# Kernel optimization log

Measured on AMD Instinct MI355X. Metric: run time of the kernel, lower is better.

The kernel has to match this reference:

```python
import jax, jax.numpy as jnp
import numpy as np

N_NODES = 50000
D_FEAT = 128
HIDDEN = 256
CLASSES = 40
N_EDGES = 800000


def setup_inputs() -> dict:
    key = jax.random.key(0)
    ks = jax.random.split(key, 8)
    x = jax.random.normal(ks[0], (N_NODES, D_FEAT), dtype=jnp.float32)
    edge_index = jax.random.randint(ks[1], (2, N_EDGES), 0, N_NODES, dtype=jnp.int64)
    s1 = 1.0 / np.sqrt(D_FEAT)
    s2 = 1.0 / np.sqrt(HIDDEN)
    # PyG SAGEConv: lin_l (applied to aggregated neighbors, has bias), lin_r (root, no bias)
    Wl1 = jax.random.uniform(ks[2], (HIDDEN, D_FEAT), jnp.float32, -s1, s1)
    bl1 = jnp.zeros((HIDDEN,), jnp.float32)
    Wr1 = jax.random.uniform(ks[3], (HIDDEN, D_FEAT), jnp.float32, -s1, s1)
    Wl2 = jax.random.uniform(ks[4], (CLASSES, HIDDEN), jnp.float32, -s2, s2)
    bl2 = jnp.zeros((CLASSES,), jnp.float32)
    Wr2 = jax.random.uniform(ks[5], (CLASSES, HIDDEN), jnp.float32, -s2, s2)
    return {"x": x, "edge_index": edge_index, "Wl1": Wl1, "bl1": bl1, "Wr1": Wr1,
            "Wl2": Wl2, "bl2": bl2, "Wr2": Wr2}


def _mean_aggregate(x, src, dst, n_nodes):
    # gather source features along edges, scatter-mean into destinations
    summed = jax.ops.segment_sum(x[src], dst, num_segments=n_nodes)  # [N, d]
    counts = jax.ops.segment_sum(jnp.ones((src.shape[0],), x.dtype), dst,
                                 num_segments=n_nodes)
    return summed / jnp.maximum(counts, 1.0)[:, None]


def _sage_conv(x, src, dst, Wl, bl, Wr):
    agg = _mean_aggregate(x, src, dst, x.shape[0])
    return agg @ Wl.T + bl + x @ Wr.T


def reference(x, edge_index, Wl1, bl1, Wr1, Wl2, bl2, Wr2):
    src, dst = edge_index[0], edge_index[1]
    h = _sage_conv(x, src, dst, Wl1, bl1, Wr1)
    h = jax.nn.relu(h)
    # F.dropout(training=self.training): eval-mode inference -> identity
    h = _sage_conv(h, src, dst, Wl2, bl2, Wr2)
    return jax.nn.log_softmax(h, axis=1)
```

## Files before the change

### kernel.cpp

```cpp
#include <hip/hip_runtime.h>
#include <hip/hip_bf16.h>
#include <math.h>

#define N_NODES 50000
#define D_FEAT  128
#define HIDDEN  256
#define CLASSES 40
#define N_EDGES 800000
#define P2S 64
#define R2S 48
#define HLS 264
#define ALS 136
#define NTILES 3125
#define GRID_L 512
#define NBUCK 196
#define BCAP  5120
#define XCVT_BLOCKS 6250
#define BA_BLOCKS 784
#define WCVT_BLOCKS 336
#define FRONT_BLOCKS (XCVT_BLOCKS + BA_BLOCKS + WCVT_BLOCKS)

typedef unsigned int  u32;
typedef unsigned short u16;
typedef __attribute__((ext_vector_type(8))) short short8;
typedef __attribute__((ext_vector_type(4))) float floatx4;

__device__ __forceinline__ float bf_lo(u32 w) { union { u32 i; float f; } u; u.i = w << 16; return u.f; }
__device__ __forceinline__ float bf_hi(u32 w) { union { u32 i; float f; } u; u.i = w & 0xffff0000u; return u.f; }
__device__ __forceinline__ float bf1(u16 h)   { union { u32 i; float f; } u; u.i = ((u32)h) << 16; return u.f; }
__device__ __forceinline__ u16 f2bf(float f) {
  union { float f; u32 i; } u; u.f = f; u32 i = u.i;
  return (u16)((i + 0x7fffu + ((i >> 16) & 1u)) >> 16);
}
__device__ __forceinline__ u32 packbf(float a, float b) { return (u32)f2bf(a) | ((u32)f2bf(b) << 16); }

__device__ __forceinline__ bool edges_are_i64(const void* eraw) {
  const long long* p = (const long long*)eraw;
  bool ok = true;
  #pragma unroll
  for (int i = 0; i < 8; i++) {
    long long v = p[(size_t)i * 100003];
    ok = ok && (v >= 0) && (v < N_NODES);
  }
  return ok;
}

__global__ __launch_bounds__(256) void front_kernel(
    const float* __restrict__ x, u16* __restrict__ xb,
    const void* __restrict__ eraw, int* __restrict__ bcur, u32* __restrict__ bbuf,
    const float* __restrict__ Wl1, const float* __restrict__ Wr1,
    const float* __restrict__ Wl2, const float* __restrict__ Wr2,
    u16* __restrict__ wb) {
  const int t = threadIdx.x;
  if (blockIdx.x < XCVT_BLOCKS) {
    int i = (blockIdx.x * 256 + t) * 4;
    floatx4 v = *(const floatx4*)(x + i);
    u32* o = (u32*)(xb + i);
    o[0] = packbf(v.x, v.y);
    o[1] = packbf(v.z, v.w);
    return;
  }
  if (blockIdx.x >= XCVT_BLOCKS + BA_BLOCKS) {
    int i = (blockIdx.x - XCVT_BLOCKS - BA_BLOCKS) * 256 + t;
    if (i < 32768)      wb[i] = f2bf(Wl1[i]);
    else if (i < 65536) wb[i] = f2bf(Wr1[i - 32768]);
    else if (i < 75776) wb[i] = f2bf(Wl2[i - 65536]);
    else if (i < 86016) wb[i] = f2bf(Wr2[i - 75776]);
    return;
  }
  __shared__ int hist[NBUCK], base[NBUCK], loc[NBUCK];
  const bool i64f = edges_are_i64(eraw);
  const int eb = blockIdx.x - XCVT_BLOCKS;
  for (int i = t; i < NBUCK; i += 256) { hist[i] = 0; loc[i] = 0; }
  __syncthreads();

  int sreg[4], dreg[4];
  const int e0 = eb * 1024;
  #pragma unroll
  for (int j = 0; j < 4; j++) {
    int e = e0 + j * 256 + t;
    int ss = 0, dd = -1;
    if (e < N_EDGES) {
      if (i64f) {
        const long long* p = (const long long*)eraw;
        ss = (int)p[e]; dd = (int)p[N_EDGES + e];
      } else {
        const int* p = (const int*)eraw;
        ss = p[e]; dd = p[N_EDGES + e];
      }
      if ((u32)ss >= N_NODES || (u32)dd >= N_NODES) dd = -1;
    }
    sreg[j] = ss; dreg[j] = dd;
    if (dd >= 0) atomicAdd(&hist[dd >> 8], 1);
  }
  __syncthreads();
  for (int i = t; i < NBUCK; i += 256)
    base[i] = atomicAdd(&bcur[i], hist[i]);
  __syncthreads();
  #pragma unroll
  for (int j = 0; j < 4; j++) {
    int dd = dreg[j];
    if (dd >= 0) {
      int bk = dd >> 8;
      int pos = base[bk] + atomicAdd(&loc[bk], 1);
      if (pos < BCAP)
        bbuf[(size_t)bk * BCAP + pos] = (u32)sreg[j] | ((u32)(dd & 255) << 16);
    }
  }
}

__global__ __launch_bounds__(256) void bucketBC_kernel(
    const u32* __restrict__ bbuf, const int* __restrict__ bcur,
    int* __restrict__ offsets, int* __restrict__ csr) {
  __shared__ int cnt[256];
  __shared__ int lds[256];
  const int t = threadIdx.x;
  const int b = blockIdx.x;
  int c196 = (t < NBUCK) ? min(bcur[t], BCAP) : 0;
  lds[t] = c196;
  __syncthreads();
  #pragma unroll
  for (int d = 1; d < 256; d <<= 1) {
    int v = (t >= d) ? lds[t - d] : 0;
    __syncthreads();
    lds[t] += v;
    __syncthreads();
  }
  const int btop = (b > 0) ? lds[b - 1] : 0;
  if (b == NBUCK - 1 && t == 0) offsets[N_NODES] = lds[NBUCK - 1];
  cnt[t] = 0;
  __syncthreads();
  const int n = min(bcur[b], BCAP);
  for (int i = t; i < n; i += 256) {
    u32 e = bbuf[(size_t)b * BCAP + i];
    atomicAdd(&cnt[(e >> 16) & 255], 1);
  }
  __syncthreads();
  int c = cnt[t];
  lds[t] = c;
  __syncthreads();
  #pragma unroll
  for (int d = 1; d < 256; d <<= 1) {
    int v = (t >= d) ? lds[t - d] : 0;
    __syncthreads();
    lds[t] += v;
    __syncthreads();
  }
  const int node = b * 256 + t;
  const int off = lds[t] - c + btop;
  if (node < N_NODES) offsets[node] = off;
  cnt[t] = off;
  __syncthreads();
  for (int i = t; i < n; i += 256) {
    u32 e = bbuf[(size_t)b * BCAP + i];
    int dl = (e >> 16) & 255;
    int pos = atomicAdd(&cnt[dl], 1);
    csr[pos] = (int)(e & 0xFFFFu);
  }
}

__global__ __launch_bounds__(256) void gather1_kernel(
    const u16* __restrict__ xb, const int* __restrict__ offsets,
    const int* __restrict__ csr_src, u16* __restrict__ agg1) {
  const int node = blockIdx.x * 4 + (threadIdx.x >> 6);
  const int lane = threadIdx.x & 63;
  int b = offsets[node], e = offsets[node + 1];
  float a0 = 0.f, a1 = 0.f, b0 = 0.f, b1 = 0.f;
  float c0 = 0.f, c1 = 0.f, d0 = 0.f, d1 = 0.f;
  float e0 = 0.f, e1 = 0.f, f0 = 0.f, f1 = 0.f;
  float g0 = 0.f, g1 = 0.f, h0 = 0.f, h1 = 0.f;
  int i = b;
  for (; i + 8 <= e; i += 8) {
    int s0 = csr_src[i],     s1 = csr_src[i + 1], s2 = csr_src[i + 2], s3 = csr_src[i + 3];
    int s4 = csr_src[i + 4], s5 = csr_src[i + 5], s6 = csr_src[i + 6], s7 = csr_src[i + 7];
    u32 w0 = ((const u32*)(xb + (size_t)s0 * D_FEAT))[lane];
    u32 w1 = ((const u32*)(xb + (size_t)s1 * D_FEAT))[lane];
    u32 w2 = ((const u32*)(xb + (size_t)s2 * D_FEAT))[lane];
    u32 w3 = ((const u32*)(xb + (size_t)s3 * D_FEAT))[lane];
    u32 w4 = ((const u32*)(xb + (size_t)s4 * D_FEAT))[lane];
    u32 w5 = ((const u32*)(xb + (size_t)s5 * D_FEAT))[lane];
    u32 w6 = ((const u32*)(xb + (size_t)s6 * D_FEAT))[lane];
    u32 w7 = ((const u32*)(xb + (size_t)s7 * D_FEAT))[lane];
    a0 += bf_lo(w0); a1 += bf_hi(w0);
    b0 += bf_lo(w1); b1 += bf_hi(w1);
    c0 += bf_lo(w2); c1 += bf_hi(w2);
    d0 += bf_lo(w3); d1 += bf_hi(w3);
    e0 += bf_lo(w4); e1 += bf_hi(w4);
    f0 += bf_lo(w5); f1 += bf_hi(w5);
    g0 += bf_lo(w6); g1 += bf_hi(w6);
    h0 += bf_lo(w7); h1 += bf_hi(w7);
  }
  for (; i < e; i++) {
    int s = csr_src[i];
    u32 w = ((const u32*)(xb + (size_t)s * D_FEAT))[lane];
    a0 += bf_lo(w); a1 += bf_hi(w);
  }
  float s0 = ((a0 + b0) + (c0 + d0)) + ((e0 + f0) + (g0 + h0));
  float s1 = ((a1 + b1) + (c1 + d1)) + ((e1 + f1) + (g1 + h1));
  float inv = 1.0f / (float)max(e - b, 1);
  ((u32*)(agg1 + (size_t)node * D_FEAT))[lane] = packbf(s0 * inv, s1 * inv);
}

__global__ __launch_bounds__(256, 2) void layer_kernel(
    const u16* __restrict__ agg1, const u16* __restrict__ xb,
    const u16* __restrict__ Wl1b, const u16* __restrict__ Wr1b,
    const float* __restrict__ bl1,
    const u16* __restrict__ Wl2b, const u16* __restrict__ Wr2b,
    const float* __restrict__ bl2,
    u16* __restrict__ p2b, float* __restrict__ r2f) {
  __shared__ u16 h_lds[16 * HLS];
  __shared__ u16 a_lds[16 * ALS];
  __shared__ u16 x_lds[16 * ALS];
  const int lane = threadIdx.x & 63;
  const int wave = threadIdx.x >> 6;
  const int n15  = lane & 15;
  const int quad = lane >> 4;
  const int ko   = quad * 8;
  const int colbase = wave * 64;
  const int srow = (wave << 2) + quad;
  const int scol = n15 * 8;

  short8 Bf[8][4];
  #pragma unroll
  for (int s = 0; s < 8; s++) {
    const u16* W = (s < 4) ? Wl1b : Wr1b;
    const int kk = (s & 3) * 32;
    #pragma unroll
    for (int t = 0; t < 4; t++)
      Bf[s][t] = *(const short8*)(W + (size_t)(colbase + t * 16 + n15) * D_FEAT + ko + kk);
  }

  const int  c0   = wave;
  const bool isR0 = (c0 >= 3);
  const int  tc0  = c0 - (isR0 ? 3 : 0);
  const int  wr0  = min(tc0 * 16 + n15, CLASSES - 1);
  const u16* Wc0  = (isR0 ? Wr2b : Wl2b) + (size_t)wr0 * HIDDEN + ko;
  const bool has1 = (wave < 2);
  const int  tc1  = wave + 1;
  const int  wr1  = min(tc1 * 16 + n15, CLASSES - 1);
  const u16* Wc1  = Wr2b + (size_t)wr1 * HIDDEN + ko;

  const float bias0 = bl2[min(tc0 * 16 + n15, CLASSES - 1)];
  const float bias1 = bl2[min(tc1 * 16 + n15, CLASSES - 1)];

  for (int tile = blockIdx.x; tile < NTILES; tile += GRID_L) {
    const int m0 = tile * 16;
    {
      const size_t g = (size_t)(m0 + srow) * D_FEAT + scol;
      *(short8*)(a_lds + srow * ALS + scol) = *(const short8*)(agg1 + g);
      *(short8*)(x_lds + srow * ALS + scol) = *(const short8*)(xb + g);
    }
    __syncthreads();
    {
      floatx4 acc[4];
      #pragma unroll
      for (int t = 0; t < 4; t++) acc[t] = floatx4{0.f, 0.f, 0.f, 0.f};

      short8 a[4];
      #pragma unroll
      for (int s = 0; s < 4; s++) a[s] = *(const short8*)(a_lds + n15 * ALS + ko + s * 32);
      #pragma unroll
      for (int s = 0; s < 4; s++)
        #pragma unroll
        for (int t = 0; t < 4; t++)
          acc[t] = __builtin_amdgcn_mfma_f32_16x16x32_bf16(a[s], Bf[s][t], acc[t], 0, 0, 0);
      #pragma unroll
      for (int s = 0; s < 4; s++) a[s] = *(const short8*)(x_lds + n15 * ALS + ko + s * 32);
      #pragma unroll
      for (int s = 0; s < 4; s++)
        #pragma unroll
        for (int t = 0; t < 4; t++)
          acc[t] = __builtin_amdgcn_mfma_f32_16x16x32_bf16(a[s], Bf[4 + s][t], acc[t], 0, 0, 0);

      #pragma unroll
      for (int t = 0; t < 4; t++) {
        int col = colbase + t * 16 + n15;
        float bias = bl1[col];
        #pragma unroll
        for (int r = 0; r < 4; r++) {
          float v = acc[t][r] + bias;
          v = v > 0.f ? v : 0.f;
          h_lds[(quad * 4 + r) * HLS + col] = f2bf(v);
        }
      }
    }
    __syncthreads();
    {
      floatx4 acc0 = floatx4{0.f, 0.f, 0.f, 0.f};
      floatx4 acc1 = floatx4{0.f, 0.f, 0.f, 0.f};
      #pragma unroll
      for (int s = 0; s < 8; s++) {
        short8 a2 = *(const short8*)(&h_lds[n15 * HLS + s * 32 + ko]);
        acc0 = __builtin_amdgcn_mfma_f32_16x16x32_bf16(a2, *(const short8*)(Wc0 + s * 32), acc0, 0, 0, 0);
        if (has1)
          acc1 = __builtin_amdgcn_mfma_f32_16x16x32_bf16(a2, *(const short8*)(Wc1 + s * 32), acc1, 0, 0, 0);
      }
      {
        int col = tc0 * 16 + n15;
        #pragma unroll
        for (int r = 0; r < 4; r++) {
          int row = m0 + quad * 4 + r;
          if (isR0) r2f[(size_t)row * R2S + col] = acc0[r] + bias0;
          else      p2b[(size_t)row * P2S + col] = f2bf(acc0[r]);
        }
      }
      if (has1) {
        int col = tc1 * 16 + n15;
        #pragma unroll
        for (int r = 0; r < 4; r++) {
          int row = m0 + quad * 4 + r;
          r2f[(size_t)row * R2S + col] = acc1[r] + bias1;
        }
      }
    }
    __syncthreads();
  }
}

__global__ __launch_bounds__(256) void final_kernel(
    const u16* __restrict__ p2b, const float* __restrict__ r2f,
    const int* __restrict__ offsets, const int* __restrict__ csr_src,
    float* __restrict__ out) {
  const int node  = blockIdx.x * 4 + (threadIdx.x >> 6);
  const int lane  = threadIdx.x & 63;
  const int eslot = lane >> 5;
  const int k     = lane & 31;
  const u32* p2w  = (const u32*)p2b;
  int b = offsets[node], e = offsets[node + 1];
  float slo = 0.f, shi = 0.f;
  int i = b;
  for (; i + 16 <= e; i += 16) {
    int c[8];
    #pragma unroll
    for (int j = 0; j < 8; j++) c[j] = csr_src[i + 2 * j + eslot];
    u32 w[8];
    #pragma unroll
    for (int j = 0; j < 8; j++) w[j] = p2w[((u32)c[j] << 5) + k];
    #pragma unroll
    for (int j = 0; j < 8; j++) { slo += bf_lo(w[j]); shi += bf_hi(w[j]); }
  }
  for (; i + 2 <= e; i += 2) {
    int c = csr_src[i + eslot];
    u32 w = p2w[((u32)c << 5) + k];
    slo += bf_lo(w); shi += bf_hi(w);
  }
  if (i < e && eslot == 0) {
    int c = csr_src[i];
    u32 w = p2w[((u32)c << 5) + k];
    slo += bf_lo(w); shi += bf_hi(w);
  }
  slo += __shfl_xor(slo, 32, 64);
  shi += __shfl_xor(shi, 32, 64);
  float vlo = __shfl(slo, lane >> 1, 64);
  float vhi = __shfl(shi, lane >> 1, 64);
  float ssum = (lane & 1) ? vhi : vlo;
  float inv = 1.0f / (float)max(e - b, 1);
  const bool act = (lane < CLASSES);
  float v = act ? (ssum * inv + r2f[(size_t)node * R2S + lane]) : -INFINITY;
  float mx = v;
  #pragma unroll
  for (int d = 1; d < 64; d <<= 1) mx = fmaxf(mx, __shfl_xor(mx, d, 64));
  float ex = act ? expf(v - mx) : 0.f;
  float sum = ex;
  #pragma unroll
  for (int d = 1; d < 64; d <<= 1) sum += __shfl_xor(sum, d, 64);
  float l = mx + logf(sum);
  if (act) out[(size_t)node * CLASSES + lane] = v - l;
}

extern "C" void kernel_launch(void* const* d_in, const int* in_sizes, int n_in,
                              void* d_out, int out_size, void* d_ws, size_t ws_size,
                              hipStream_t stream) {
  const float* x   = (const float*)d_in[0];
  const void*  ei  = d_in[1];
  const float* Wl1 = (const float*)d_in[2];
  const float* bl1 = (const float*)d_in[3];
  const float* Wr1 = (const float*)d_in[4];
  const float* Wl2 = (const float*)d_in[5];
  const float* bl2 = (const float*)d_in[6];
  const float* Wr2 = (const float*)d_in[7];

  char* ws = (char*)d_ws;
  size_t off = 0;
  int* csr       = (int*)(ws + off); off += (size_t)N_EDGES * 4;
  int* offsets   = (int*)(ws + off); off += 204800;
  int* bcur      = (int*)(ws + off); off += 1024;
  u32* bbuf      = (u32*)(ws + off); off += (size_t)NBUCK * BCAP * 4;
  u16* wb        = (u16*)(ws + off); off += 172288;
  u16* xb        = (u16*)(ws + off); off += (size_t)N_NODES * D_FEAT * 2;
  u16* agg1      = (u16*)(ws + off); off += (size_t)N_NODES * D_FEAT * 2;
  u16* p2b       = (u16*)(ws + off); off += (size_t)N_NODES * P2S * 2;
  float* r2f     = (float*)(ws + off); off += (size_t)N_NODES * R2S * 4;

  u16* Wl1b = wb;
  u16* Wr1b = wb + 32768;
  u16* Wl2b = wb + 65536;
  u16* Wr2b = wb + 75776;

  hipMemsetAsync(bcur, 0, NBUCK * 4, stream);
  front_kernel<<<FRONT_BLOCKS, 256, 0, stream>>>(x, xb, ei, bcur, bbuf,
                                                 Wl1, Wr1, Wl2, Wr2, wb);
  bucketBC_kernel<<<NBUCK, 256, 0, stream>>>(bbuf, bcur, offsets, csr);
  gather1_kernel<<<N_NODES / 4, 256, 0, stream>>>(xb, offsets, csr, agg1);
  layer_kernel<<<GRID_L, 256, 0, stream>>>(agg1, xb, Wl1b, Wr1b, bl1,
                                           Wl2b, Wr2b, bl2, p2b, r2f);
  final_kernel<<<N_NODES / 4, 256, 0, stream>>>(p2b, r2f, offsets, csr, (float*)d_out);
}
```

Measured before the change: 220.7 us.

## Split layer-2 projection into 32+8 column arrays to cut gather bytes

The projected layer-2 neighbor features used to be stored as 64 bf16 columns per row, even though only 40 are meaningful. They are now stored in two dense arrays: a 64-byte row for columns 0-31 and a 16-byte row for columns 32-39. The final gather kernel reads each edge with 16 lanes from the main array, plus 4 lanes from the side array, handling 4 edges per wavefront step. This cuts padding bytes fetched per edge in the random gather, at the cost of a second scattered access per edge, extra shuffles, and divergent side-lane loads.

```diff
diff --git a/kernel.cpp b/kernel.cpp
--- a/kernel.cpp
+++ b/kernel.cpp
@@ -6,8 +6,6 @@
 #define D_FEAT  128
 #define HIDDEN  256
 #define CLASSES 40
-#define N_EDGES 800000
-#define P2S 64
 #define R2S 48
 #define HLS 264
 #define ALS 136
@@ -15,6 +13,7 @@
 #define GRID_L 512
 #define NBUCK 196
 #define BCAP  5120
+#define N_EDGES 800000
 #define XCVT_BLOCKS 6250
 #define BA_BLOCKS 784
 #define WCVT_BLOCKS 336
@@ -207,7 +206,7 @@
     const float* __restrict__ bl1,
     const u16* __restrict__ Wl2b, const u16* __restrict__ Wr2b,
     const float* __restrict__ bl2,
-    u16* __restrict__ p2b, float* __restrict__ r2f) {
+    u16* __restrict__ p2a, u16* __restrict__ p2c, float* __restrict__ r2f) {
   __shared__ u16 h_lds[16 * HLS];
   __shared__ u16 a_lds[16 * ALS];
   __shared__ u16 x_lds[16 * ALS];
@@ -300,8 +299,13 @@
         #pragma unroll
         for (int r = 0; r < 4; r++) {
           int row = m0 + quad * 4 + r;
-          if (isR0) r2f[(size_t)row * R2S + col] = acc0[r] + bias0;
-          else      p2b[(size_t)row * P2S + col] = f2bf(acc0[r]);
+          if (isR0) {
+            r2f[(size_t)row * R2S + col] = acc0[r] + bias0;
+          } else if (col < 32) {
+            p2a[(size_t)row * 32 + col] = f2bf(acc0[r]);
+          } else if (col < CLASSES) {
+            p2c[(size_t)row * 8 + (col - 32)] = f2bf(acc0[r]);
+          }
         }
       }
       if (has1) {
@@ -318,42 +322,62 @@
 }
 
 __global__ __launch_bounds__(256) void final_kernel(
-    const u16* __restrict__ p2b, const float* __restrict__ r2f,
+    const u16* __restrict__ p2a, const u16* __restrict__ p2c,
+    const float* __restrict__ r2f,
     const int* __restrict__ offsets, const int* __restrict__ csr_src,
     float* __restrict__ out) {
   const int node  = blockIdx.x * 4 + (threadIdx.x >> 6);
   const int lane  = threadIdx.x & 63;
-  const int eslot = lane >> 5;
-  const int k     = lane & 31;
-  const u32* p2w  = (const u32*)p2b;
+  const int eslot = lane >> 4;
+  const int k     = lane & 15;
+  const bool side = (k < 4);
+  const u32* pa = (const u32*)p2a;
+  const u32* pc = (const u32*)p2c;
   int b = offsets[node], e = offsets[node + 1];
   float slo = 0.f, shi = 0.f;
+  float tlo = 0.f, thi = 0.f;
   int i = b;
   for (; i + 16 <= e; i += 16) {
-    int c[8];
+    int c[4];
     #pragma unroll
-    for (int j = 0; j < 8; j++) c[j] = csr_src[i + 2 * j + eslot];
-    u32 w[8];
+    for (int j = 0; j < 4; j++) c[j] = csr_src[i + 4 * j + eslot];
+    u32 w[4];
     #pragma unroll
-    for (int j = 0; j < 8; j++) w[j] = p2w[((u32)c[j] << 5) + k];
+    for (int j = 0; j < 4; j++) w[j] = pa[((u32)c[j] << 4) + k];
+    if (side) {
+      u32 v[4];
+      #pragma unroll
+      for (int j = 0; j < 4; j++) v[j] = pc[((u32)c[j] << 2) + k];
+      #pragma unroll
+      for (int j = 0; j < 4; j++) { tlo += bf_lo(v[j]); thi += bf_hi(v[j]); }
+    }
     #pragma unroll
-    for (int j = 0; j < 8; j++) { slo += bf_lo(w[j]); shi += bf_hi(w[j]); }
-  }
-  for (; i + 2 <= e; i += 2) {
+    for (int j = 0; j < 4; j++) { slo += bf_lo(w[j]); shi += bf_hi(w[j]); }
+  }
+  for (; i + 4 <= e; i += 4) {
     int c = csr_src[i + eslot];
-    u32 w = p2w[((u32)c << 5) + k];
+    u32 w = pa[((u32)c << 4) + k];
     slo += bf_lo(w); shi += bf_hi(w);
-  }
-  if (i < e && eslot == 0) {
-    int c = csr_src[i];
-    u32 w = p2w[((u32)c << 5) + k];
+    if (side) { u32 v = pc[((u32)c << 2) + k]; tlo += bf_lo(v); thi += bf_hi(v); }
+  }
+  if (i < e && eslot < (e - i)) {
+    int c = csr_src[i + eslot];
+    u32 w = pa[((u32)c << 4) + k];
     slo += bf_lo(w); shi += bf_hi(w);
-  }
-  slo += __shfl_xor(slo, 32, 64);
-  shi += __shfl_xor(shi, 32, 64);
-  float vlo = __shfl(slo, lane >> 1, 64);
-  float vhi = __shfl(shi, lane >> 1, 64);
-  float ssum = (lane & 1) ? vhi : vlo;
+    if (side) { u32 v = pc[((u32)c << 2) + k]; tlo += bf_lo(v); thi += bf_hi(v); }
+  }
+  slo += __shfl_xor(slo, 16, 64); slo += __shfl_xor(slo, 32, 64);
+  shi += __shfl_xor(shi, 16, 64); shi += __shfl_xor(shi, 32, 64);
+  tlo += __shfl_xor(tlo, 16, 64); tlo += __shfl_xor(tlo, 32, 64);
+  thi += __shfl_xor(thi, 16, 64); thi += __shfl_xor(thi, 32, 64);
+  const int src = (lane >> 1) & 15;
+  float vl = __shfl(slo, src, 64);
+  float vh = __shfl(shi, src, 64);
+  float ul = __shfl(tlo, src, 64);
+  float uh = __shfl(thi, src, 64);
+  float mlo = (lane < 32) ? vl : ul;
+  float mhi = (lane < 32) ? vh : uh;
+  float ssum = (lane & 1) ? mhi : mlo;
   float inv = 1.0f / (float)max(e - b, 1);
   const bool act = (lane < CLASSES);
   float v = act ? (ssum * inv + r2f[(size_t)node * R2S + lane]) : -INFINITY;
@@ -389,7 +413,8 @@
   u16* wb        = (u16*)(ws + off); off += 172288;
   u16* xb        = (u16*)(ws + off); off += (size_t)N_NODES * D_FEAT * 2;
   u16* agg1      = (u16*)(ws + off); off += (size_t)N_NODES * D_FEAT * 2;
-  u16* p2b       = (u16*)(ws + off); off += (size_t)N_NODES * P2S * 2;
+  u16* p2a       = (u16*)(ws + off); off += (size_t)N_NODES * 32 * 2;
+  u16* p2c       = (u16*)(ws + off); off += (size_t)N_NODES * 8 * 2;
   float* r2f     = (float*)(ws + off); off += (size_t)N_NODES * R2S * 4;
 
   u16* Wl1b = wb;
@@ -403,6 +428,6 @@
   bucketBC_kernel<<<NBUCK, 256, 0, stream>>>(bbuf, bcur, offsets, csr);
   gather1_kernel<<<N_NODES / 4, 256, 0, stream>>>(xb, offsets, csr, agg1);
   layer_kernel<<<GRID_L, 256, 0, stream>>>(agg1, xb, Wl1b, Wr1b, bl1,
-                                           Wl2b, Wr2b, bl2, p2b, r2f);
-  final_kernel<<<N_NODES / 4, 256, 0, stream>>>(p2b, r2f, offsets, csr, (float*)d_out);
-}
+                                           Wl2b, Wr2b, bl2, p2a, p2c, r2f);
+  final_kernel<<<N_NODES / 4, 256, 0, stream>>>(p2a, p2c, r2f, offsets, csr, (float*)d_out);
+}
```

Result: no change. 218.4 us (-1.1%).
